# Optimization experiments

Measured on AMD Instinct MI355X. Metric: run time of the kernel, lower is better.

The kernel has to match this reference:

```python
import jax, jax.numpy as jnp
import numpy as np

B, L, D_MODEL = 2, 1024, 1024
D_STATE, D_CONV, EXPAND = 16, 4, 2
D_INNER = D_MODEL * EXPAND
LN_EPS = 1e-5


def setup_inputs() -> dict:
    key = jax.random.key(0)
    ks = jax.random.split(key, 6)
    g = lambda k, shape, scale: (jax.random.normal(k, shape, jnp.float32) * scale)
    x = jax.random.normal(ks[0], (B, L, D_MODEL), jnp.float32)
    in_proj_w = g(ks[1], (2 * D_INNER, D_MODEL), D_MODEL ** -0.5)
    conv_w = g(ks[2], (D_INNER, D_CONV), D_CONV ** -0.5)   # depthwise kernel
    conv_b = jnp.zeros((D_INNER,), jnp.float32)
    x_proj_w = g(ks[3], (2 * D_STATE + 1, D_INNER), D_INNER ** -0.5)
    A_log = jnp.tile(jnp.log(jnp.arange(1, D_STATE + 1, dtype=jnp.float32)), (D_INNER, 1))
    D_param = jnp.ones((D_INNER,), jnp.float32)
    dt_w = g(ks[4], (D_INNER, 1), 1.0)
    dt_b = jnp.full((D_INNER,), -4.0, jnp.float32)
    out_w = g(ks[5], (D_MODEL, D_INNER), D_INNER ** -0.5)
    ln_g = jnp.ones((D_INNER,), jnp.float32)
    ln_b = jnp.zeros((D_INNER,), jnp.float32)
    return dict(x=x, in_proj_w=in_proj_w, conv_w=conv_w, conv_b=conv_b,
                x_proj_w=x_proj_w, A_log=A_log, D_param=D_param,
                dt_w=dt_w, dt_b=dt_b, out_w=out_w, ln_g=ln_g, ln_b=ln_b)


def _forward(x, in_proj_w, conv_w, conv_b, x_proj_w, A_log, D_param,
             dt_w, dt_b, out_w, ln_g, ln_b):
    Lq = x.shape[1]
    xz = jnp.einsum('bld,ed->ble', x, in_proj_w)            # (B,L,2*Di)
    xb, z = xz[..., :D_INNER], xz[..., D_INNER:]
    # causal depthwise conv1d (pad left d_conv-1, valid conv == torch pad+truncate)
    xpad = jnp.pad(xb, ((0, 0), (D_CONV - 1, 0), (0, 0)))
    xc = conv_b
    for k in range(D_CONV):
        xc = xc + xpad[:, k:k + Lq, :] * conv_w[:, k]
    xb = jax.nn.silu(xc)
    proj = jnp.einsum('bld,ed->ble', xb, x_proj_w)          # (B,L,2N+1)
    dt_in = proj[..., :1]
    Bp = proj[..., 1:1 + D_STATE]                            # (B,L,N)
    Cp = proj[..., 1 + D_STATE:]                             # (B,L,N)
    dt = jax.nn.softplus(dt_in * dt_w[:, 0] + dt_b)          # (B,L,Di)
    A = -jnp.exp(A_log)                                      # (Di,N)
    dA = jnp.exp(dt[..., None] * A)                          # (B,L,Di,N)
    x_scaled = (xb * dt)[..., None] * Bp[..., None, :]       # (B,L,Di,N)
    # linear recurrence h[t] = dA[t]*h[t-1] + x_scaled[t] via associative scan
    def comb(a, b):
        return (a[0] * b[0], b[0] * a[1] + b[1])
    _, h = jax.lax.associative_scan(comb, (dA, x_scaled), axis=1)
    y = jnp.einsum('bldn,bln->bld', h, Cp) + xb * D_param    # (B,L,Di)
    mu = jnp.mean(y, axis=-1, keepdims=True)
    var = jnp.var(y, axis=-1, keepdims=True)
    y = (y - mu) / jnp.sqrt(var + LN_EPS) * ln_g + ln_b
    y = y * jax.nn.silu(z)
    return jnp.einsum('bld,ed->ble', y, out_w)               # (B,L,d_model)


def reference(x, in_proj_w, conv_w, conv_b, x_proj_w, A_log, D_param,
              dt_w, dt_b, out_w, ln_g, ln_b):
    return _forward(x, in_proj_w, conv_w, conv_b, x_proj_w, A_log, D_param,
                    dt_w, dt_b, out_w, ln_g, ln_b)
```

## Files before the change

### kernel.cpp

```cpp
#include <hip/hip_runtime.h>

typedef unsigned short u16;
typedef unsigned int u32;
typedef __bf16 bf16x8 __attribute__((ext_vector_type(8)));
typedef float f32x4 __attribute__((ext_vector_type(4)));

__device__ __forceinline__ float bf2f(u16 b) {
    return __uint_as_float(((u32)b) << 16);
}
__device__ __forceinline__ u16 f2bf(float f) {
    u32 u = __float_as_uint(f);
    return (u16)((u + 0x7fffu + ((u >> 16) & 1u)) >> 16);
}

#define P_CONVW 0
#define P_CONVB 8192
#define P_ALOG  10240
#define P_DPAR  43008
#define P_DTW   45056
#define P_DTB   47104
#define P_LNG   49152
#define P_LNB   51200
#define P_TOTAL 53248

#define CCH 32
#define CT  32
#define CHUNKTOT 2097152
#define PSTRIDE 128

struct ParamPtrs { const void* p[8]; };

__global__ __launch_bounds__(256) void canon_params(ParamPtrs pp, float* __restrict__ dst,
                                                    const u16* __restrict__ dp) {
    const bool isbf = (dp[0] != 0);
    const int i = blockIdx.x * 256 + threadIdx.x;
    int seg, off;
    if (i < P_CONVB)      { seg = 0; off = i; }
    else if (i < P_ALOG)  { seg = 1; off = i - P_CONVB; }
    else if (i < P_DPAR)  { seg = 2; off = i - P_ALOG; }
    else if (i < P_DTW)   { seg = 3; off = i - P_DPAR; }
    else if (i < P_DTB)   { seg = 4; off = i - P_DTW; }
    else if (i < P_LNG)   { seg = 5; off = i - P_DTB; }
    else if (i < P_LNB)   { seg = 6; off = i - P_LNG; }
    else                  { seg = 7; off = i - P_LNB; }
    dst[i] = isbf ? bf2f(((const u16*)pp.p[seg])[off]) : ((const float*)pp.p[seg])[off];
}

#define CV_X   524288
#define CV_W1  1572864
#define CV_TOT 2097152
__global__ __launch_bounds__(256) void canon_multi(const void* __restrict__ sx,
                                                   const void* __restrict__ sw1,
                                                   const void* __restrict__ swo,
                                                   u16* __restrict__ dst,
                                                   const u16* __restrict__ dp) {
    const bool isbf = (dp[0] != 0);
    const int i = blockIdx.x * 256 + threadIdx.x;
    if (i >= CV_TOT) return;
    const void* src;
    int off;
    if (i < CV_X)       { src = sx;  off = i; }
    else if (i < CV_W1) { src = sw1; off = i - CV_X; }
    else                { src = swo; off = i - CV_W1; }
    if (isbf) {
        ((uint2*)dst)[i] = ((const uint2*)src)[off];
    } else {
        const float4 v = ((const float4*)src)[off];
        uint2 o;
        o.x = (u32)f2bf(v.x) | ((u32)f2bf(v.y) << 16);
        o.y = (u32)f2bf(v.z) | ((u32)f2bf(v.w) << 16);
        ((uint2*)dst)[i] = o;
    }
}

__global__ __launch_bounds__(256) void canon_wpad(const void* __restrict__ src,
                                                  u16* __restrict__ dst,
                                                  const u16* __restrict__ dp) {
    const bool isbf = (dp[0] != 0);
    const int i = blockIdx.x * 256 + threadIdx.x;
    const int idx = i * 4;
    const int row = idx >> 11;
    u16 o[4];
#pragma unroll
    for (int q = 0; q < 4; ++q) {
        float v = 0.f;
        if (row < 33)
            v = isbf ? bf2f(((const u16*)src)[idx + q]) : ((const float*)src)[idx + q];
        o[q] = f2bf(v);
    }
    *(uint2*)&dst[idx] = *(uint2*)o;
}

template <bool STORE_F32>
__global__ __launch_bounds__(256) void gemm_bt(const u16* __restrict__ A,
                                               const u16* __restrict__ Bw,
                                               void* __restrict__ C,
                                               int M, int N, int Kseg,
                                               int lda, int ldb) {
    const int bm = blockIdx.x;
    const int bn = blockIdx.y;
    const int kbase = blockIdx.z * Kseg;
    const int tid = threadIdx.x;
    const int lane = tid & 63;
    const int wave = tid >> 6;
    const int wm = wave >> 1, wn = wave & 1;
    const int l16 = lane & 15, quad = lane >> 4;

    __shared__ __align__(16) u16 sA[128 * 32];
    __shared__ __align__(16) u16 sB[128 * 32];

    f32x4 acc[4][4] = {};

    const int rsub = lane >> 2;
    const int csub = (lane & 3) * 8;

    for (int k0 = 0; k0 < Kseg; k0 += 32) {
        const int kc = kbase + k0 + csub;
        __syncthreads();
#pragma unroll
        for (int q = 0; q < 2; ++q) {
            const int g = wave + 4 * q;
            const int row = g * 16 + rsub;
            __builtin_amdgcn_global_load_lds(
                (const u32*)&A[(size_t)(bm * 128 + row) * lda + kc],
                (u32*)&sA[g * 512], 16, 0, 0);
            __builtin_amdgcn_global_load_lds(
                (const u32*)&Bw[(size_t)(bn * 128 + row) * ldb + kc],
                (u32*)&sB[g * 512], 16, 0, 0);
        }
        __syncthreads();

        bf16x8 af[4], bg[4];
#pragma unroll
        for (int t = 0; t < 4; ++t) {
            af[t] = *(const bf16x8*)&sA[(wm * 64 + t * 16 + l16) * 32 + quad * 8];
            bg[t] = *(const bf16x8*)&sB[(wn * 64 + t * 16 + l16) * 32 + quad * 8];
        }
#pragma unroll
        for (int mt = 0; mt < 4; ++mt)
#pragma unroll
            for (int nt = 0; nt < 4; ++nt)
                acc[mt][nt] = __builtin_amdgcn_mfma_f32_16x16x32_bf16(
                    af[mt], bg[nt], acc[mt][nt], 0, 0, 0);
    }

    float* Cf = (float*)C + (size_t)blockIdx.z * M * N;
#pragma unroll
    for (int mt = 0; mt < 4; ++mt) {
#pragma unroll
        for (int r = 0; r < 4; ++r) {
            const int row = bm * 128 + wm * 64 + mt * 16 + quad * 4 + r;
#pragma unroll
            for (int nt = 0; nt < 4; ++nt) {
                const int col = bn * 128 + wn * 64 + nt * 16 + l16;
                if (STORE_F32)
                    Cf[(size_t)row * N + col] = acc[mt][nt][r];
                else
                    ((u16*)C)[(size_t)row * N + col] = f2bf(acc[mt][nt][r]);
            }
        }
    }
}

__global__ __launch_bounds__(256) void reduce_parts(const float* __restrict__ src,
                                                    float* __restrict__ dst,
                                                    int n4, int parts) {
    const int i = blockIdx.x * 256 + threadIdx.x;
    if (i >= n4) return;
    float4 s = ((const float4*)src)[i];
    for (int p = 1; p < parts; ++p) {
        const float4 v = ((const float4*)src)[(size_t)p * n4 + i];
        s.x += v.x; s.y += v.y; s.z += v.z; s.w += v.w;
    }
    ((float4*)dst)[i] = s;
}

__global__ __launch_bounds__(256) void conv_silu(const u16* __restrict__ xz,
                                                 const float* __restrict__ par,
                                                 u16* __restrict__ xb16) {
    const int idx = blockIdx.x * 256 + threadIdx.x;
    const int d = idx & 2047;
    const int bl = idx >> 11;
    const int l = bl & 1023;
    float acc = par[P_CONVB + d];
#pragma unroll
    for (int k = 0; k < 4; ++k) {
        const int ls = l + k - 3;
        if (ls >= 0)
            acc = fmaf(bf2f(xz[(size_t)(bl + (ls - l)) * 4096 + d]),
                       par[P_CONVW + d * 4 + k], acc);
    }
    const float s = acc / (1.f + __expf(-acc));
    xb16[idx] = f2bf(s);
}

__global__ __launch_bounds__(256) void scan_p1(const u16* __restrict__ xb16,
                                               const float* __restrict__ proj,
                                               const float* __restrict__ par,
                                               float* __restrict__ PS) {
    const int d = blockIdx.x * 256 + threadIdx.x;
    const int c = blockIdx.y;
    const int b = blockIdx.z;
    __shared__ float sp[CT][33];
    const size_t row0 = (size_t)b * 1024 + c * CT;
    for (int f = threadIdx.x; f < CT * 33; f += 256) {
        const int i = f / 33, j = f - i * 33;
        sp[i][j] = proj[(row0 + i) * PSTRIDE + j];
    }
    float Aneg[16];
#pragma unroll
    for (int n = 0; n < 16; ++n) Aneg[n] = -__expf(par[P_ALOG + d * 16 + n]);
    const float dtw = par[P_DTW + d], dtb = par[P_DTB + d];
    __syncthreads();

    float h[16] = {}, P[16];
#pragma unroll
    for (int n = 0; n < 16; ++n) P[n] = 1.f;

    float xv = bf2f(xb16[row0 * 2048 + d]);
    for (int i = 0; i < CT; ++i) {
        const float xv_next = (i + 1 < CT) ? bf2f(xb16[(row0 + i + 1) * 2048 + d]) : 0.f;
        const float dtin = sp[i][0];
        const float darg = fmaf(dtin, dtw, dtb);
        const float dt = (darg > 20.f) ? darg : __logf(1.f + __expf(darg));
        const float xdt = xv * dt;
#pragma unroll
        for (int n = 0; n < 16; ++n) {
            const float dA = __expf(dt * Aneg[n]);
            P[n] *= dA;
            h[n] = fmaf(dA, h[n], xdt * sp[i][1 + n]);
        }
        xv = xv_next;
    }
    const size_t base = (((size_t)b * CCH + c) * 16) * 2048 + d;
#pragma unroll
    for (int n = 0; n < 16; ++n) {
        PS[base + (size_t)n * 2048] = P[n];
        PS[CHUNKTOT + base + (size_t)n * 2048] = h[n];
    }
}

__global__ __launch_bounds__(256) void scan_comb(const float* __restrict__ PS,
                                                 float* __restrict__ H) {
    const int t = blockIdx.x * 256 + threadIdx.x;
    const int d = t & 2047;
    const int n = (t >> 11) & 15;
    const int b = t >> 15;
    float h = 0.f;
#pragma unroll
    for (int c = 0; c < CCH; ++c) {
        const size_t idx = (((size_t)b * CCH + c) * 16 + n) * 2048 + d;
        H[idx] = h;
        h = fmaf(PS[idx], h, PS[CHUNKTOT + idx]);
    }
}

__global__ __launch_bounds__(256) void scan_p2(const u16* __restrict__ xb16,
                                               const float* __restrict__ proj,
                                               const float* __restrict__ par,
                                               const float* __restrict__ H,
                                               u16* __restrict__ y) {
    const int d = blockIdx.x * 256 + threadIdx.x;
    const int c = blockIdx.y;
    const int b = blockIdx.z;
    __shared__ float sp[CT][33];
    const size_t row0 = (size_t)b * 1024 + c * CT;
    for (int f = threadIdx.x; f < CT * 33; f += 256) {
        const int i = f / 33, j = f - i * 33;
        sp[i][j] = proj[(row0 + i) * PSTRIDE + j];
    }
    float Aneg[16], h[16];
    const size_t hbase = (((size_t)b * CCH + c) * 16) * 2048 + d;
#pragma unroll
    for (int n = 0; n < 16; ++n) {
        Aneg[n] = -__expf(par[P_ALOG + d * 16 + n]);
        h[n] = H[hbase + (size_t)n * 2048];
    }
    const float dtw = par[P_DTW + d], dtb = par[P_DTB + d];
    const float Dp = par[P_DPAR + d];
    __syncthreads();

    float xv = bf2f(xb16[row0 * 2048 + d]);
    for (int i = 0; i < CT; ++i) {
        const float xv_next = (i + 1 < CT) ? bf2f(xb16[(row0 + i + 1) * 2048 + d]) : 0.f;
        const float dtin = sp[i][0];
        const float darg = fmaf(dtin, dtw, dtb);
        const float dt = (darg > 20.f) ? darg : __logf(1.f + __expf(darg));
        const float xdt = xv * dt;
        float acc = 0.f;
#pragma unroll
        for (int n = 0; n < 16; ++n) {
            const float dA = __expf(dt * Aneg[n]);
            h[n] = fmaf(dA, h[n], xdt * sp[i][1 + n]);
            acc = fmaf(h[n], sp[i][17 + n], acc);
        }
        y[(row0 + i) * 2048 + d] = f2bf(fmaf(xv, Dp, acc));
        xv = xv_next;
    }
}

__global__ __launch_bounds__(256) void ln_silu(const u16* __restrict__ y,
                                               const u16* __restrict__ xz,
                                               const float* __restrict__ par,
                                               u16* __restrict__ yn) {
    const int row = blockIdx.x;
    const int tid = threadIdx.x;
    const int lane = tid & 63, wave = tid >> 6;
    float v[8];
    float s = 0.f, s2 = 0.f;
#pragma unroll
    for (int i = 0; i < 8; ++i) {
        v[i] = bf2f(y[(size_t)row * 2048 + tid + i * 256]);
        s += v[i];
        s2 = fmaf(v[i], v[i], s2);
    }
    s += __shfl_xor(s, 1); s2 += __shfl_xor(s2, 1);
    s += __shfl_xor(s, 2); s2 += __shfl_xor(s2, 2);
    s += __shfl_xor(s, 4); s2 += __shfl_xor(s2, 4);
    s += __shfl_xor(s, 8); s2 += __shfl_xor(s2, 8);
    s += __shfl_xor(s, 16); s2 += __shfl_xor(s2, 16);
    s += __shfl_xor(s, 32); s2 += __shfl_xor(s2, 32);
    __shared__ float rs[4], rs2[4];
    if (lane == 0) { rs[wave] = s; rs2[wave] = s2; }
    __syncthreads();
    const float ts = rs[0] + rs[1] + rs[2] + rs[3];
    const float ts2 = rs2[0] + rs2[1] + rs2[2] + rs2[3];
    const float mu = ts * (1.f / 2048.f);
    const float var = ts2 * (1.f / 2048.f) - mu * mu;
    const float rstd = rsqrtf(var + 1e-5f);
#pragma unroll
    for (int i = 0; i < 8; ++i) {
        const int d = tid + i * 256;
        float t = (v[i] - mu) * rstd * par[P_LNG + d] + par[P_LNB + d];
        const float z = bf2f(xz[(size_t)row * 4096 + 2048 + d]);
        t *= z / (1.f + __expf(-z));
        yn[(size_t)row * 2048 + d] = f2bf(t);
    }
}

extern "C" void kernel_launch(void* const* d_in, const int* in_sizes, int n_in,
                              void* d_out, int out_size, void* d_ws, size_t ws_size,
                              hipStream_t stream) {
    const void* x         = d_in[0];
    const void* in_proj_w = d_in[1];
    const void* conv_w    = d_in[2];
    const void* conv_b    = d_in[3];
    const void* x_proj_w  = d_in[4];
    const void* A_log     = d_in[5];
    const void* D_param   = d_in[6];
    const void* dt_w      = d_in[7];
    const void* dt_b      = d_in[8];
    const void* out_w     = d_in[9];
    const void* ln_g      = d_in[10];
    const void* ln_b      = d_in[11];
    const u16* dp = (const u16*)D_param;

    float* cpar = (float*)d_ws;
    u16* cx     = (u16*)(cpar + P_TOTAL);
    u16* cw1    = cx + 2097152;
    u16* cwo    = cw1 + 4194304;
    u16* xz     = cwo + 2097152;
    u16* xb16   = xz + 8388608;
    u16* y      = xb16 + 4194304;
    u16* wpad   = y + 4194304;
    float* proj = (float*)(wpad + 262144);
    float* PS   = proj + 262144;
    float* H    = PS + 2 * CHUNKTOT;
    float* xpart = (float*)cx;
    float* gpart = PS;
    u16* yn      = xb16;

    ParamPtrs pp;
    pp.p[0] = conv_w; pp.p[1] = conv_b; pp.p[2] = A_log; pp.p[3] = D_param;
    pp.p[4] = dt_w;   pp.p[5] = dt_b;   pp.p[6] = ln_g;  pp.p[7] = ln_b;
    canon_params<<<P_TOTAL / 256, 256, 0, stream>>>(pp, cpar, dp);
    canon_multi<<<CV_TOT / 256, 256, 0, stream>>>(x, in_proj_w, out_w, cx, dp);
    canon_wpad<<<256, 256, 0, stream>>>(x_proj_w, wpad, dp);

    gemm_bt<false><<<dim3(16, 32, 1), 256, 0, stream>>>(cx, cw1, xz, 2048, 4096, 1024, 1024, 1024);
    conv_silu<<<16384, 256, 0, stream>>>(xz, cpar, xb16);
    gemm_bt<true><<<dim3(16, 1, 8), 256, 0, stream>>>(xb16, wpad, xpart, 2048, 128, 256, 2048, 2048);
    reduce_parts<<<256, 256, 0, stream>>>(xpart, proj, 65536, 8);
    scan_p1<<<dim3(8, CCH, 2), 256, 0, stream>>>(xb16, proj, cpar, PS);
    scan_comb<<<256, 256, 0, stream>>>(PS, H);
    scan_p2<<<dim3(8, CCH, 2), 256, 0, stream>>>(xb16, proj, cpar, H, y);
    ln_silu<<<2048, 256, 0, stream>>>(y, xz, cpar, yn);
    gemm_bt<true><<<dim3(16, 8, 2), 256, 0, stream>>>(yn, cwo, gpart, 2048, 1024, 1024, 2048, 2048);
    reduce_parts<<<2048, 256, 0, stream>>>(gpart, (float*)d_out, 524288, 2);
}
```

Baseline: 256.1 us.

## Shrink GEMM tile to 64x128 and vectorize conv_silu and ln_silu accesses

The GEMM block tile drops from 128x128 to 64x128, with each wave owning a 64x32 strip, and the grids double in M so more workgroups run on the GPU's many CUs. conv_silu now handles 8 channels per thread with 128-bit loads and stores, and ln_silu reads y and z and writes yn as contiguous 8-element vectors. The smaller tile lowers reuse per block, since each B tile is loaded for half as many rows. The vectorization targets memory-bound elementwise kernels that were making scalar 16-bit accesses.

```diff
diff --git a/kernel.cpp b/kernel.cpp
--- a/kernel.cpp
+++ b/kernel.cpp
@@ -103,43 +103,42 @@
     const int tid = threadIdx.x;
     const int lane = tid & 63;
     const int wave = tid >> 6;
-    const int wm = wave >> 1, wn = wave & 1;
     const int l16 = lane & 15, quad = lane >> 4;
 
-    __shared__ __align__(16) u16 sA[128 * 32];
+    __shared__ __align__(16) u16 sA[64 * 32];
     __shared__ __align__(16) u16 sB[128 * 32];
 
-    f32x4 acc[4][4] = {};
+    f32x4 acc[4][2] = {};
 
     const int rsub = lane >> 2;
     const int csub = (lane & 3) * 8;
 
+    const u16* Arow = &A[(size_t)(bm * 64 + wave * 16 + rsub) * lda + csub];
+    const u16* Brow0 = &Bw[(size_t)(bn * 128 + wave * 16 + rsub) * ldb + csub];
+    const u16* Brow1 = &Bw[(size_t)(bn * 128 + (wave + 4) * 16 + rsub) * ldb + csub];
+    u32* sAd = (u32*)&sA[wave * 512];
+    u32* sBd0 = (u32*)&sB[wave * 512];
+    u32* sBd1 = (u32*)&sB[(wave + 4) * 512];
+
     for (int k0 = 0; k0 < Kseg; k0 += 32) {
-        const int kc = kbase + k0 + csub;
+        const int kc = kbase + k0;
         __syncthreads();
-#pragma unroll
-        for (int q = 0; q < 2; ++q) {
-            const int g = wave + 4 * q;
-            const int row = g * 16 + rsub;
-            __builtin_amdgcn_global_load_lds(
-                (const u32*)&A[(size_t)(bm * 128 + row) * lda + kc],
-                (u32*)&sA[g * 512], 16, 0, 0);
-            __builtin_amdgcn_global_load_lds(
-                (const u32*)&Bw[(size_t)(bn * 128 + row) * ldb + kc],
-                (u32*)&sB[g * 512], 16, 0, 0);
-        }
+        __builtin_amdgcn_global_load_lds((const u32*)(Arow + kc), sAd, 16, 0, 0);
+        __builtin_amdgcn_global_load_lds((const u32*)(Brow0 + kc), sBd0, 16, 0, 0);
+        __builtin_amdgcn_global_load_lds((const u32*)(Brow1 + kc), sBd1, 16, 0, 0);
         __syncthreads();
 
-        bf16x8 af[4], bg[4];
-#pragma unroll
-        for (int t = 0; t < 4; ++t) {
-            af[t] = *(const bf16x8*)&sA[(wm * 64 + t * 16 + l16) * 32 + quad * 8];
-            bg[t] = *(const bf16x8*)&sB[(wn * 64 + t * 16 + l16) * 32 + quad * 8];
-        }
+        bf16x8 af[4], bg[2];
+#pragma unroll
+        for (int t = 0; t < 4; ++t)
+            af[t] = *(const bf16x8*)&sA[(t * 16 + l16) * 32 + quad * 8];
+#pragma unroll
+        for (int t = 0; t < 2; ++t)
+            bg[t] = *(const bf16x8*)&sB[(wave * 32 + t * 16 + l16) * 32 + quad * 8];
 #pragma unroll
         for (int mt = 0; mt < 4; ++mt)
 #pragma unroll
-            for (int nt = 0; nt < 4; ++nt)
+            for (int nt = 0; nt < 2; ++nt)
                 acc[mt][nt] = __builtin_amdgcn_mfma_f32_16x16x32_bf16(
                     af[mt], bg[nt], acc[mt][nt], 0, 0, 0);
     }
@@ -149,10 +148,10 @@
     for (int mt = 0; mt < 4; ++mt) {
 #pragma unroll
         for (int r = 0; r < 4; ++r) {
-            const int row = bm * 128 + wm * 64 + mt * 16 + quad * 4 + r;
-#pragma unroll
-            for (int nt = 0; nt < 4; ++nt) {
-                const int col = bn * 128 + wn * 64 + nt * 16 + l16;
+            const int row = bm * 64 + mt * 16 + quad * 4 + r;
+#pragma unroll
+            for (int nt = 0; nt < 2; ++nt) {
+                const int col = bn * 128 + wave * 32 + nt * 16 + l16;
                 if (STORE_F32)
                     Cf[(size_t)row * N + col] = acc[mt][nt][r];
                 else
@@ -178,20 +177,31 @@
 __global__ __launch_bounds__(256) void conv_silu(const u16* __restrict__ xz,
                                                  const float* __restrict__ par,
                                                  u16* __restrict__ xb16) {
-    const int idx = blockIdx.x * 256 + threadIdx.x;
-    const int d = idx & 2047;
-    const int bl = idx >> 11;
+    const int t = blockIdx.x * 256 + threadIdx.x;
+    const int dg = (t & 255) * 8;
+    const int bl = t >> 8;
     const int l = bl & 1023;
-    float acc = par[P_CONVB + d];
+    float acc[8];
+#pragma unroll
+    for (int j = 0; j < 8; ++j) acc[j] = par[P_CONVB + dg + j];
 #pragma unroll
     for (int k = 0; k < 4; ++k) {
         const int ls = l + k - 3;
-        if (ls >= 0)
-            acc = fmaf(bf2f(xz[(size_t)(bl + (ls - l)) * 4096 + d]),
-                       par[P_CONVW + d * 4 + k], acc);
-    }
-    const float s = acc / (1.f + __expf(-acc));
-    xb16[idx] = f2bf(s);
+        if (ls >= 0) {
+            const uint4 v = *(const uint4*)&xz[(size_t)(bl + k - 3) * 4096 + dg];
+            const u16* xv = (const u16*)&v;
+#pragma unroll
+            for (int j = 0; j < 8; ++j)
+                acc[j] = fmaf(bf2f(xv[j]), par[P_CONVW + (dg + j) * 4 + k], acc[j]);
+        }
+    }
+    u16 o[8];
+#pragma unroll
+    for (int j = 0; j < 8; ++j) {
+        const float s = acc[j] / (1.f + __expf(-acc[j]));
+        o[j] = f2bf(s);
+    }
+    *(uint4*)&xb16[(size_t)bl * 2048 + dg] = *(uint4*)o;
 }
 
 __global__ __launch_bounds__(256) void scan_p1(const u16* __restrict__ xb16,
@@ -306,11 +316,14 @@
     const int row = blockIdx.x;
     const int tid = threadIdx.x;
     const int lane = tid & 63, wave = tid >> 6;
+    const int dg = tid * 8;
+    const uint4 vv = *(const uint4*)&y[(size_t)row * 2048 + dg];
+    const u16* vu = (const u16*)&vv;
     float v[8];
     float s = 0.f, s2 = 0.f;
 #pragma unroll
     for (int i = 0; i < 8; ++i) {
-        v[i] = bf2f(y[(size_t)row * 2048 + tid + i * 256]);
+        v[i] = bf2f(vu[i]);
         s += v[i];
         s2 = fmaf(v[i], v[i], s2);
     }
@@ -328,14 +341,18 @@
     const float mu = ts * (1.f / 2048.f);
     const float var = ts2 * (1.f / 2048.f) - mu * mu;
     const float rstd = rsqrtf(var + 1e-5f);
+    const uint4 zz = *(const uint4*)&xz[(size_t)row * 4096 + 2048 + dg];
+    const u16* zu = (const u16*)&zz;
+    u16 o[8];
 #pragma unroll
     for (int i = 0; i < 8; ++i) {
-        const int d = tid + i * 256;
+        const int d = dg + i;
         float t = (v[i] - mu) * rstd * par[P_LNG + d] + par[P_LNB + d];
-        const float z = bf2f(xz[(size_t)row * 4096 + 2048 + d]);
+        const float z = bf2f(zu[i]);
         t *= z / (1.f + __expf(-z));
-        yn[(size_t)row * 2048 + d] = f2bf(t);
-    }
+        o[i] = f2bf(t);
+    }
+    *(uint4*)&yn[(size_t)row * 2048 + dg] = *(uint4*)o;
 }
 
 extern "C" void kernel_launch(void* const* d_in, const int* in_sizes, int n_in,
@@ -377,14 +394,14 @@
     canon_multi<<<CV_TOT / 256, 256, 0, stream>>>(x, in_proj_w, out_w, cx, dp);
     canon_wpad<<<256, 256, 0, stream>>>(x_proj_w, wpad, dp);
 
-    gemm_bt<false><<<dim3(16, 32, 1), 256, 0, stream>>>(cx, cw1, xz, 2048, 4096, 1024, 1024, 1024);
-    conv_silu<<<16384, 256, 0, stream>>>(xz, cpar, xb16);
-    gemm_bt<true><<<dim3(16, 1, 8), 256, 0, stream>>>(xb16, wpad, xpart, 2048, 128, 256, 2048, 2048);
+    gemm_bt<false><<<dim3(32, 32, 1), 256, 0, stream>>>(cx, cw1, xz, 2048, 4096, 1024, 1024, 1024);
+    conv_silu<<<2048, 256, 0, stream>>>(xz, cpar, xb16);
+    gemm_bt<true><<<dim3(32, 1, 8), 256, 0, stream>>>(xb16, wpad, xpart, 2048, 128, 256, 2048, 2048);
     reduce_parts<<<256, 256, 0, stream>>>(xpart, proj, 65536, 8);
     scan_p1<<<dim3(8, CCH, 2), 256, 0, stream>>>(xb16, proj, cpar, PS);
     scan_comb<<<256, 256, 0, stream>>>(PS, H);
     scan_p2<<<dim3(8, CCH, 2), 256, 0, stream>>>(xb16, proj, cpar, H, y);
     ln_silu<<<2048, 256, 0, stream>>>(y, xz, cpar, yn);
-    gemm_bt<true><<<dim3(16, 8, 2), 256, 0, stream>>>(yn, cwo, gpart, 2048, 1024, 1024, 2048, 2048);
+    gemm_bt<true><<<dim3(32, 8, 2), 256, 0, stream>>>(yn, cwo, gpart, 2048, 1024, 1024, 2048, 2048);
     reduce_parts<<<2048, 256, 0, stream>>>(gpart, (float*)d_out, 524288, 2);
 }
```

Measured after the change: 266.1 us. 3.9% more time.

## Merge canon kernels, vectorize conv and layernorm, raise out-proj split-K

Applied to the files above, without the earlier changes.

Merges the three canonicalization kernels into one launch to save launch overhead. Vectorizes conv_silu and ln_silu so each thread handles 8 contiguous bf16 channels with 16-byte loads and stores. Raises the output GEMM split-K from 2 to 4 and moves its partial buffer to a dedicated region so more blocks run at once, at the cost of extra reduction traffic. The gpart buffer now sits after H and needs more workspace.

```diff
diff --git a/kernel.cpp b/kernel.cpp
--- a/kernel.cpp
+++ b/kernel.cpp
@@ -28,67 +28,68 @@
 #define CHUNKTOT 2097152
 #define PSTRIDE 128
 
+#define CV_X    524288
+#define CV_W1   1572864
+#define CV_TOT  2097152
+#define CW_PAD  65536
+#define CANON_TOT (P_TOTAL + CV_TOT + CW_PAD)
+
 struct ParamPtrs { const void* p[8]; };
 
-__global__ __launch_bounds__(256) void canon_params(ParamPtrs pp, float* __restrict__ dst,
-                                                    const u16* __restrict__ dp) {
+__global__ __launch_bounds__(256) void canon_all(ParamPtrs pp,
+                                                 const void* __restrict__ sx,
+                                                 const void* __restrict__ sw1,
+                                                 const void* __restrict__ swo,
+                                                 const void* __restrict__ swx,
+                                                 float* __restrict__ dpar,
+                                                 u16* __restrict__ dbf,
+                                                 u16* __restrict__ dwpad,
+                                                 const u16* __restrict__ dp) {
     const bool isbf = (dp[0] != 0);
-    const int i = blockIdx.x * 256 + threadIdx.x;
-    int seg, off;
-    if (i < P_CONVB)      { seg = 0; off = i; }
-    else if (i < P_ALOG)  { seg = 1; off = i - P_CONVB; }
-    else if (i < P_DPAR)  { seg = 2; off = i - P_ALOG; }
-    else if (i < P_DTW)   { seg = 3; off = i - P_DPAR; }
-    else if (i < P_DTB)   { seg = 4; off = i - P_DTW; }
-    else if (i < P_LNG)   { seg = 5; off = i - P_DTB; }
-    else if (i < P_LNB)   { seg = 6; off = i - P_LNG; }
-    else                  { seg = 7; off = i - P_LNB; }
-    dst[i] = isbf ? bf2f(((const u16*)pp.p[seg])[off]) : ((const float*)pp.p[seg])[off];
-}
-
-#define CV_X   524288
-#define CV_W1  1572864
-#define CV_TOT 2097152
-__global__ __launch_bounds__(256) void canon_multi(const void* __restrict__ sx,
-                                                   const void* __restrict__ sw1,
-                                                   const void* __restrict__ swo,
-                                                   u16* __restrict__ dst,
-                                                   const u16* __restrict__ dp) {
-    const bool isbf = (dp[0] != 0);
-    const int i = blockIdx.x * 256 + threadIdx.x;
-    if (i >= CV_TOT) return;
-    const void* src;
-    int off;
-    if (i < CV_X)       { src = sx;  off = i; }
-    else if (i < CV_W1) { src = sw1; off = i - CV_X; }
-    else                { src = swo; off = i - CV_W1; }
-    if (isbf) {
-        ((uint2*)dst)[i] = ((const uint2*)src)[off];
+    const int t = blockIdx.x * 256 + threadIdx.x;
+    if (t >= CANON_TOT) return;
+    if (t < P_TOTAL) {
+        const int i = t;
+        int seg, off;
+        if (i < P_CONVB)      { seg = 0; off = i; }
+        else if (i < P_ALOG)  { seg = 1; off = i - P_CONVB; }
+        else if (i < P_DPAR)  { seg = 2; off = i - P_ALOG; }
+        else if (i < P_DTW)   { seg = 3; off = i - P_DPAR; }
+        else if (i < P_DTB)   { seg = 4; off = i - P_DTW; }
+        else if (i < P_LNG)   { seg = 5; off = i - P_DTB; }
+        else if (i < P_LNB)   { seg = 6; off = i - P_LNG; }
+        else                  { seg = 7; off = i - P_LNB; }
+        dpar[i] = isbf ? bf2f(((const u16*)pp.p[seg])[off]) : ((const float*)pp.p[seg])[off];
+    } else if (t < P_TOTAL + CV_TOT) {
+        const int i = t - P_TOTAL;
+        const void* src;
+        int off;
+        if (i < CV_X)       { src = sx;  off = i; }
+        else if (i < CV_W1) { src = sw1; off = i - CV_X; }
+        else                { src = swo; off = i - CV_W1; }
+        if (isbf) {
+            ((uint2*)dbf)[i] = ((const uint2*)src)[off];
+        } else {
+            const float4 v = ((const float4*)src)[off];
+            uint2 o;
+            o.x = (u32)f2bf(v.x) | ((u32)f2bf(v.y) << 16);
+            o.y = (u32)f2bf(v.z) | ((u32)f2bf(v.w) << 16);
+            ((uint2*)dbf)[i] = o;
+        }
     } else {
-        const float4 v = ((const float4*)src)[off];
-        uint2 o;
-        o.x = (u32)f2bf(v.x) | ((u32)f2bf(v.y) << 16);
-        o.y = (u32)f2bf(v.z) | ((u32)f2bf(v.w) << 16);
-        ((uint2*)dst)[i] = o;
-    }
-}
-
-__global__ __launch_bounds__(256) void canon_wpad(const void* __restrict__ src,
-                                                  u16* __restrict__ dst,
-                                                  const u16* __restrict__ dp) {
-    const bool isbf = (dp[0] != 0);
-    const int i = blockIdx.x * 256 + threadIdx.x;
-    const int idx = i * 4;
-    const int row = idx >> 11;
-    u16 o[4];
-#pragma unroll
-    for (int q = 0; q < 4; ++q) {
-        float v = 0.f;
-        if (row < 33)
-            v = isbf ? bf2f(((const u16*)src)[idx + q]) : ((const float*)src)[idx + q];
-        o[q] = f2bf(v);
-    }
-    *(uint2*)&dst[idx] = *(uint2*)o;
+        const int i = t - P_TOTAL - CV_TOT;
+        const int idx = i * 4;
+        const int row = idx >> 11;
+        u16 o[4];
+#pragma unroll
+        for (int q = 0; q < 4; ++q) {
+            float v = 0.f;
+            if (row < 33)
+                v = isbf ? bf2f(((const u16*)swx)[idx + q]) : ((const float*)swx)[idx + q];
+            o[q] = f2bf(v);
+        }
+        *(uint2*)&dwpad[idx] = *(uint2*)o;
+    }
 }
 
 template <bool STORE_F32>
@@ -178,20 +179,31 @@
 __global__ __launch_bounds__(256) void conv_silu(const u16* __restrict__ xz,
                                                  const float* __restrict__ par,
                                                  u16* __restrict__ xb16) {
-    const int idx = blockIdx.x * 256 + threadIdx.x;
-    const int d = idx & 2047;
-    const int bl = idx >> 11;
+    const int t = blockIdx.x * 256 + threadIdx.x;
+    const int dg = (t & 255) * 8;
+    const int bl = t >> 8;
     const int l = bl & 1023;
-    float acc = par[P_CONVB + d];
+    float acc[8];
+#pragma unroll
+    for (int j = 0; j < 8; ++j) acc[j] = par[P_CONVB + dg + j];
 #pragma unroll
     for (int k = 0; k < 4; ++k) {
         const int ls = l + k - 3;
-        if (ls >= 0)
-            acc = fmaf(bf2f(xz[(size_t)(bl + (ls - l)) * 4096 + d]),
-                       par[P_CONVW + d * 4 + k], acc);
-    }
-    const float s = acc / (1.f + __expf(-acc));
-    xb16[idx] = f2bf(s);
+        if (ls >= 0) {
+            const uint4 v = *(const uint4*)&xz[(size_t)(bl + k - 3) * 4096 + dg];
+            const u16* xv = (const u16*)&v;
+#pragma unroll
+            for (int j = 0; j < 8; ++j)
+                acc[j] = fmaf(bf2f(xv[j]), par[P_CONVW + (dg + j) * 4 + k], acc[j]);
+        }
+    }
+    u16 o[8];
+#pragma unroll
+    for (int j = 0; j < 8; ++j) {
+        const float s = acc[j] / (1.f + __expf(-acc[j]));
+        o[j] = f2bf(s);
+    }
+    *(uint4*)&xb16[(size_t)bl * 2048 + dg] = *(uint4*)o;
 }
 
 __global__ __launch_bounds__(256) void scan_p1(const u16* __restrict__ xb16,
@@ -306,11 +318,14 @@
     const int row = blockIdx.x;
     const int tid = threadIdx.x;
     const int lane = tid & 63, wave = tid >> 6;
+    const int dg = tid * 8;
+    const uint4 vv = *(const uint4*)&y[(size_t)row * 2048 + dg];
+    const u16* vu = (const u16*)&vv;
     float v[8];
     float s = 0.f, s2 = 0.f;
 #pragma unroll
     for (int i = 0; i < 8; ++i) {
-        v[i] = bf2f(y[(size_t)row * 2048 + tid + i * 256]);
+        v[i] = bf2f(vu[i]);
         s += v[i];
         s2 = fmaf(v[i], v[i], s2);
     }
@@ -328,14 +343,18 @@
     const float mu = ts * (1.f / 2048.f);
     const float var = ts2 * (1.f / 2048.f) - mu * mu;
     const float rstd = rsqrtf(var + 1e-5f);
+    const uint4 zz = *(const uint4*)&xz[(size_t)row * 4096 + 2048 + dg];
+    const u16* zu = (const u16*)&zz;
+    u16 o[8];
 #pragma unroll
     for (int i = 0; i < 8; ++i) {
-        const int d = tid + i * 256;
+        const int d = dg + i;
         float t = (v[i] - mu) * rstd * par[P_LNG + d] + par[P_LNB + d];
-        const float z = bf2f(xz[(size_t)row * 4096 + 2048 + d]);
+        const float z = bf2f(zu[i]);
         t *= z / (1.f + __expf(-z));
-        yn[(size_t)row * 2048 + d] = f2bf(t);
-    }
+        o[i] = f2bf(t);
+    }
+    *(uint4*)&yn[(size_t)row * 2048 + dg] = *(uint4*)o;
 }
 
 extern "C" void kernel_launch(void* const* d_in, const int* in_sizes, int n_in,
@@ -366,25 +385,24 @@
     float* proj = (float*)(wpad + 262144);
     float* PS   = proj + 262144;
     float* H    = PS + 2 * CHUNKTOT;
+    float* gpart = H + CHUNKTOT;
     float* xpart = (float*)cx;
-    float* gpart = PS;
     u16* yn      = xb16;
 
     ParamPtrs pp;
     pp.p[0] = conv_w; pp.p[1] = conv_b; pp.p[2] = A_log; pp.p[3] = D_param;
     pp.p[4] = dt_w;   pp.p[5] = dt_b;   pp.p[6] = ln_g;  pp.p[7] = ln_b;
-    canon_params<<<P_TOTAL / 256, 256, 0, stream>>>(pp, cpar, dp);
-    canon_multi<<<CV_TOT / 256, 256, 0, stream>>>(x, in_proj_w, out_w, cx, dp);
-    canon_wpad<<<256, 256, 0, stream>>>(x_proj_w, wpad, dp);
+    canon_all<<<(CANON_TOT + 255) / 256, 256, 0, stream>>>(
+        pp, x, in_proj_w, out_w, x_proj_w, cpar, cx, wpad, dp);
 
     gemm_bt<false><<<dim3(16, 32, 1), 256, 0, stream>>>(cx, cw1, xz, 2048, 4096, 1024, 1024, 1024);
-    conv_silu<<<16384, 256, 0, stream>>>(xz, cpar, xb16);
+    conv_silu<<<2048, 256, 0, stream>>>(xz, cpar, xb16);
     gemm_bt<true><<<dim3(16, 1, 8), 256, 0, stream>>>(xb16, wpad, xpart, 2048, 128, 256, 2048, 2048);
     reduce_parts<<<256, 256, 0, stream>>>(xpart, proj, 65536, 8);
     scan_p1<<<dim3(8, CCH, 2), 256, 0, stream>>>(xb16, proj, cpar, PS);
     scan_comb<<<256, 256, 0, stream>>>(PS, H);
     scan_p2<<<dim3(8, CCH, 2), 256, 0, stream>>>(xb16, proj, cpar, H, y);
     ln_silu<<<2048, 256, 0, stream>>>(y, xz, cpar, yn);
-    gemm_bt<true><<<dim3(16, 8, 2), 256, 0, stream>>>(yn, cwo, gpart, 2048, 1024, 1024, 2048, 2048);
-    reduce_parts<<<2048, 256, 0, stream>>>(gpart, (float*)d_out, 524288, 2);
-}
+    gemm_bt<true><<<dim3(16, 8, 4), 256, 0, stream>>>(yn, cwo, gpart, 2048, 1024, 512, 2048, 2048);
+    reduce_parts<<<2048, 256, 0, stream>>>(gpart, (float*)d_out, 524288, 4);
+}
```

Result: no change. 257.2 us (+0.4%).
